# Optimization experiments

Hardware: AMD Instinct MI355X
Metric: run time of the kernel (lower is better)

Reference implementation:

```python
import jax, jax.numpy as jnp
import numpy as np

EPS = 1e-9
B, A = 16, 8400
N = B * A


def _make_boxes(key, shape):
    # valid xyxy boxes inside a 640x640 canvas
    k1, k2 = jax.random.split(key)
    xy1 = jax.random.uniform(k1, shape, dtype=jnp.float32) * 600.0
    wh = jax.random.uniform(k2, shape, dtype=jnp.float32) * 100.0 + 1.0
    return jnp.concatenate([xy1, xy1 + wh], axis=-1)  # [..., 4]


def setup_inputs() -> dict:
    key = jax.random.key(0)
    kp, kt, kn = jax.random.split(key, 3)
    predicts_bbox = _make_boxes(kp, (B, A, 2))
    targets_bbox = _make_boxes(kt, (B, A, 2))
    valid_masks = jnp.ones((B, A), dtype=bool)
    box_norm = jax.random.uniform(kn, (N,), dtype=jnp.float32)
    cls_norm = jnp.asarray(float(N), dtype=jnp.float32)
    return {
        "predicts_bbox": predicts_bbox,
        "targets_bbox": targets_bbox,
        "valid_masks": valid_masks,
        "box_norm": box_norm,
        "cls_norm": cls_norm,
    }


def _ciou_diag(b1, b2):
    # b1, b2: [N, 4] xyxy. Per-pair CIoU == diag of the pairwise matrix in the
    # original calculate_iou, computed directly in O(N).
    x1a, y1a, x2a, y2a = b1[:, 0], b1[:, 1], b1[:, 2], b1[:, 3]
    x1b, y1b, x2b, y2b = b2[:, 0], b2[:, 1], b2[:, 2], b2[:, 3]

    xmin = jnp.maximum(x1a, x1b)
    ymin = jnp.maximum(y1a, y1b)
    xmax = jnp.minimum(x2a, x2b)
    ymax = jnp.minimum(y2a, y2b)
    inter = jnp.clip(xmax - xmin, 0.0) * jnp.clip(ymax - ymin, 0.0)

    area_a = (x2a - x1a) * (y2a - y1a)
    area_b = (x2b - x1b) * (y2b - y1b)
    union = area_a + area_b - inter
    iou = inter / (union + EPS)

    # center distance squared
    cx = (x1a + x2a - x1b - x2b) * 0.5
    cy = (y1a + y2a - y1b - y2b) * 0.5
    cent2 = cx * cx + cy * cy

    # enclosing box diagonal squared
    cw = jnp.maximum(x2a, x2b) - jnp.minimum(x1a, x1b)
    ch = jnp.maximum(y2a, y2b) - jnp.minimum(y1a, y1b)
    diag2 = cw * cw + ch * ch

    diou = iou - cent2 / (diag2 + EPS)

    # aspect-ratio consistency term
    wa, ha = x2a - x1a, y2a - y1a
    wb, hb = x2b - x1b, y2b - y1b
    arctan = jnp.arctan(wa / (ha + EPS)) - jnp.arctan(wb / (hb + EPS))
    v = (4.0 / (jnp.pi ** 2)) * arctan * arctan
    alpha = v / (v - iou + 1.0 + EPS)
    return diou - alpha * v


def reference(predicts_bbox, targets_bbox, valid_masks, box_norm, cls_norm):
    p = predicts_bbox.reshape(-1, 4)
    t = targets_bbox.reshape(-1, 4)
    m = valid_masks.reshape(-1).astype(p.dtype)
    iou = _ciou_diag(p, t)
    loss_iou = (1.0 - iou) * m  # mask is all-True -> identical to boolean gather
    return (loss_iou * box_norm).sum() / cls_norm
```

## Files before the change

kernel.cpp:

```cpp
#include <hip/hip_runtime.h>
#include <hip/hip_bf16.h>
#include <math.h>

#define EPS 1e-9f
#define FOUR_OVER_PI2 0.40528473456935108578f

#define BLOCK 256
#define ITER 4

__device__ __forceinline__ float ciou_loss_elem(float4 a, float4 b,
                                                int mval, float bn)
{
    float x1a = a.x, y1a = a.y, x2a = a.z, y2a = a.w;
    float x1b = b.x, y1b = b.y, x2b = b.z, y2b = b.w;

    float xmin = fmaxf(x1a, x1b);
    float ymin = fmaxf(y1a, y1b);
    float xmax = fminf(x2a, x2b);
    float ymax = fminf(y2a, y2b);

    float iw = fmaxf(xmax - xmin, 0.0f);
    float ih = fmaxf(ymax - ymin, 0.0f);
    float inter = iw * ih;

    float wa = x2a - x1a, ha = y2a - y1a;
    float wb = x2b - x1b, hb = y2b - y1b;

    float area_a = wa * ha;
    float area_b = wb * hb;
    float uni = area_a + area_b - inter;
    float iou = inter / (uni + EPS);

    float cx = (x1a + x2a - x1b - x2b) * 0.5f;
    float cy = (y1a + y2a - y1b - y2b) * 0.5f;
    float cent2 = cx * cx + cy * cy;

    float cw = fmaxf(x2a, x2b) - fminf(x1a, x1b);
    float ch = fmaxf(y2a, y2b) - fminf(y1a, y1b);
    float diag2 = cw * cw + ch * ch;

    float diou = iou - cent2 / (diag2 + EPS);

    float at = atanf(wa / (ha + EPS)) - atanf(wb / (hb + EPS));
    float v = FOUR_OVER_PI2 * at * at;
    float alpha = v / (v - iou + 1.0f + EPS);
    float ciou = diou - alpha * v;

    float m = (mval != 0) ? 1.0f : 0.0f;
    return (1.0f - ciou) * m * bn;
}

__global__ __launch_bounds__(BLOCK) void ciou_partial_kernel(
    const float4* __restrict__ pb,
    const float4* __restrict__ tb,
    const int* __restrict__ mask,
    const float* __restrict__ box_norm,
    float* __restrict__ partials,
    int n)
{
    int tid = blockIdx.x * BLOCK + threadIdx.x;
    int stride = gridDim.x * BLOCK;

    float local = 0.0f;
    #pragma unroll
    for (int it = 0; it < ITER; ++it) {
        int i = tid + it * stride;
        if (i < n) {
            local += ciou_loss_elem(pb[i], tb[i], mask[i], box_norm[i]);
        }
    }

    #pragma unroll
    for (int off = 32; off > 0; off >>= 1)
        local += __shfl_down(local, off, 64);

    __shared__ float smem[BLOCK / 64];
    int lane = threadIdx.x & 63;
    int wid  = threadIdx.x >> 6;
    if (lane == 0) smem[wid] = local;
    __syncthreads();

    if (threadIdx.x == 0) {
        float s = smem[0] + smem[1] + smem[2] + smem[3];
        partials[blockIdx.x] = s;
    }
}

__global__ __launch_bounds__(BLOCK) void ciou_final_kernel(
    const float* __restrict__ partials,
    const float* __restrict__ cls_norm,
    float* __restrict__ out,
    int nparts)
{
    float local = (threadIdx.x < nparts) ? partials[threadIdx.x] : 0.0f;

    #pragma unroll
    for (int off = 32; off > 0; off >>= 1)
        local += __shfl_down(local, off, 64);

    __shared__ float smem[BLOCK / 64];
    int lane = threadIdx.x & 63;
    int wid  = threadIdx.x >> 6;
    if (lane == 0) smem[wid] = local;
    __syncthreads();

    if (threadIdx.x == 0) {
        float s = smem[0] + smem[1] + smem[2] + smem[3];
        out[0] = s / cls_norm[0];
    }
}

extern "C" void kernel_launch(void* const* d_in, const int* in_sizes, int n_in,
                              void* d_out, int out_size, void* d_ws, size_t ws_size,
                              hipStream_t stream) {
    const float4* pb       = (const float4*)d_in[0];
    const float4* tb       = (const float4*)d_in[1];
    const int*    mask     = (const int*)d_in[2];
    const float*  box_norm = (const float*)d_in[3];
    const float*  cls_norm = (const float*)d_in[4];
    float* out      = (float*)d_out;
    float* partials = (float*)d_ws;

    int n = in_sizes[3];

    int grid = (n + BLOCK * ITER - 1) / (BLOCK * ITER);

    ciou_partial_kernel<<<grid, BLOCK, 0, stream>>>(pb, tb, mask, box_norm, partials, n);
    ciou_final_kernel<<<1, BLOCK, 0, stream>>>(partials, cls_norm, out, grid);
}
```

Measured before the change: 10.86 us.

## Fuse partial and final reductions via cooperative grid sync, vectorize mask/norm loads

Merges the two-kernel reduction into one cooperative kernel that writes per-block partials, does a grid-wide sync, and lets block 0 finish the sum and divide by cls_norm. Each thread now handles four contiguous elements and loads mask and box_norm as int4/float4 vectors. This is meant to remove a second kernel launch and to widen the small loads. In exchange it pays for a grid barrier and relies on the cooperative launch. The new code also assumes n is divisible by 4, and its final step only reads up to 256 partials.

```diff
diff --git a/kernel.cpp b/kernel.cpp
--- a/kernel.cpp
+++ b/kernel.cpp
@@ -1,12 +1,14 @@
 #include <hip/hip_runtime.h>
 #include <hip/hip_bf16.h>
+#include <hip/hip_cooperative_groups.h>
 #include <math.h>
+
+namespace cg = cooperative_groups;
 
 #define EPS 1e-9f
 #define FOUR_OVER_PI2 0.40528473456935108578f
 
 #define BLOCK 256
-#define ITER 4
 
 __device__ __forceinline__ float ciou_loss_elem(float4 a, float4 b,
                                                 int mval, float bn)
@@ -50,24 +52,28 @@
     return (1.0f - ciou) * m * bn;
 }
 
-__global__ __launch_bounds__(BLOCK) void ciou_partial_kernel(
+__global__ __launch_bounds__(BLOCK) void ciou_fused_kernel(
     const float4* __restrict__ pb,
     const float4* __restrict__ tb,
-    const int* __restrict__ mask,
-    const float* __restrict__ box_norm,
+    const int4* __restrict__ mask4,
+    const float4* __restrict__ bn4,
+    const float* __restrict__ cls_norm,
+    float* __restrict__ out,
     float* __restrict__ partials,
-    int n)
+    int ngroups,
+    int nparts)
 {
-    int tid = blockIdx.x * BLOCK + threadIdx.x;
-    int stride = gridDim.x * BLOCK;
+    int g = blockIdx.x * BLOCK + threadIdx.x;
 
     float local = 0.0f;
-    #pragma unroll
-    for (int it = 0; it < ITER; ++it) {
-        int i = tid + it * stride;
-        if (i < n) {
-            local += ciou_loss_elem(pb[i], tb[i], mask[i], box_norm[i]);
-        }
+    if (g < ngroups) {
+        int4   mv = mask4[g];
+        float4 bn = bn4[g];
+        int base = g * 4;
+        local  = ciou_loss_elem(pb[base + 0], tb[base + 0], mv.x, bn.x);
+        local += ciou_loss_elem(pb[base + 1], tb[base + 1], mv.y, bn.y);
+        local += ciou_loss_elem(pb[base + 2], tb[base + 2], mv.z, bn.z);
+        local += ciou_loss_elem(pb[base + 3], tb[base + 3], mv.w, bn.w);
     }
 
     #pragma unroll
@@ -81,32 +87,26 @@
     __syncthreads();
 
     if (threadIdx.x == 0) {
-        float s = smem[0] + smem[1] + smem[2] + smem[3];
-        partials[blockIdx.x] = s;
+        partials[blockIdx.x] = smem[0] + smem[1] + smem[2] + smem[3];
     }
-}
 
-__global__ __launch_bounds__(BLOCK) void ciou_final_kernel(
-    const float* __restrict__ partials,
-    const float* __restrict__ cls_norm,
-    float* __restrict__ out,
-    int nparts)
-{
-    float local = (threadIdx.x < nparts) ? partials[threadIdx.x] : 0.0f;
+    cg::this_grid().sync();
 
-    #pragma unroll
-    for (int off = 32; off > 0; off >>= 1)
-        local += __shfl_down(local, off, 64);
+    if (blockIdx.x == 0) {
+        float v = (threadIdx.x < nparts) ? partials[threadIdx.x] : 0.0f;
 
-    __shared__ float smem[BLOCK / 64];
-    int lane = threadIdx.x & 63;
-    int wid  = threadIdx.x >> 6;
-    if (lane == 0) smem[wid] = local;
-    __syncthreads();
+        #pragma unroll
+        for (int off = 32; off > 0; off >>= 1)
+            v += __shfl_down(v, off, 64);
 
-    if (threadIdx.x == 0) {
-        float s = smem[0] + smem[1] + smem[2] + smem[3];
-        out[0] = s / cls_norm[0];
+        __shared__ float smem2[BLOCK / 64];
+        if (lane == 0) smem2[wid] = v;
+        __syncthreads();
+
+        if (threadIdx.x == 0) {
+            float s = smem2[0] + smem2[1] + smem2[2] + smem2[3];
+            out[0] = s / cls_norm[0];
+        }
     }
 }
 
@@ -115,16 +115,18 @@
                               hipStream_t stream) {
     const float4* pb       = (const float4*)d_in[0];
     const float4* tb       = (const float4*)d_in[1];
-    const int*    mask     = (const int*)d_in[2];
-    const float*  box_norm = (const float*)d_in[3];
+    const int4*   mask4    = (const int4*)d_in[2];
+    const float4* bn4      = (const float4*)d_in[3];
     const float*  cls_norm = (const float*)d_in[4];
     float* out      = (float*)d_out;
     float* partials = (float*)d_ws;
 
     int n = in_sizes[3];
+    int ngroups = n / 4;
+    int grid = (ngroups + BLOCK - 1) / BLOCK;
 
-    int grid = (n + BLOCK * ITER - 1) / (BLOCK * ITER);
-
-    ciou_partial_kernel<<<grid, BLOCK, 0, stream>>>(pb, tb, mask, box_norm, partials, n);
-    ciou_final_kernel<<<1, BLOCK, 0, stream>>>(partials, cls_norm, out, grid);
+    void* args[] = { &pb, &tb, &mask4, &bn4, &cls_norm, &out, &partials,
+                     &ngroups, &grid };
+    hipLaunchCooperativeKernel((const void*)ciou_fused_kernel,
+                               dim3(grid), dim3(BLOCK), args, 0, stream);
 }
```

New measurement: 40.41 us. 272% more time.
